# Kernel optimization log

Measured on AMD Instinct MI355X. Metric: run time of the kernel, lower is better.

Reference implementation:

```python
import jax, jax.numpy as jnp
import numpy as np

N, L, M, NNZ, P, G, H = 4096, 64, 256, 100000, 3, 1, 8
D = M // H  # head_dim = 32


def setup_inputs() -> dict:
    key = jax.random.key(0)
    ks = jax.random.split(key, 8)
    return {
        "sparse_values": jax.random.normal(ks[0], (NNZ, M), jnp.float32),
        "linear_index": jax.random.randint(ks[1], (N, L), 0, NNZ, jnp.int32),
        "is_specified": jax.random.randint(ks[2], (N, L), 0, 2, jnp.int32).astype(bool),
        "query": jax.random.normal(ks[3], (N, M), jnp.float32),
        "key_weight": jax.random.normal(ks[4], (M, M), jnp.float32) * 0.05,
        "value_weight": jax.random.normal(ks[5], (M, M), jnp.float32) * 0.05,
        "key_positions": jax.random.uniform(ks[6], (N, L, P), jnp.float32),
        "rope_freqs": jax.random.normal(ks[7], (P, G, H, D // 2), jnp.float32),
        "n_heads": H,
    }


def reference(sparse_values, linear_index, is_specified, query, key_weight,
              value_weight, key_positions, rope_freqs, n_heads):
    n, l = linear_index.shape
    m = query.shape[-1]
    h = n_heads
    d = m // h
    scale = 1.0 / np.sqrt(m)  # docstring: default scale_factor = 1/sqrt(M)

    # Gather each query's key subset; unspecified keys -> 0 (will be masked)
    safe_idx = jnp.where(is_specified, linear_index, 0)
    gathered = jnp.where(is_specified[..., None], sparse_values[safe_idx], 0.0)  # [N,L,M]

    # Key / value projections (nn.Linear convention: x @ W.T)
    k = (gathered @ key_weight.T).reshape(n, l, h, d)
    v = (gathered @ value_weight.T).reshape(n, l, h, d)

    # RoPE on keys: angles [N,L,H,D/2], summed over position dims P and freq groups G
    angles = jnp.einsum('nlp,pghd->nlhd', key_positions, rope_freqs)
    cos, sin = jnp.cos(angles), jnp.sin(angles)
    k_even, k_odd = k[..., 0::2], k[..., 1::2]
    k = jnp.stack([k_even * cos - k_odd * sin,
                   k_even * sin + k_odd * cos], axis=-1).reshape(n, l, h, d)

    # Per-query subset attention (query is pre-rotated per docstring)
    q = query.reshape(n, h, d)
    scores = jnp.einsum('nhd,nlhd->nhl', q, k) * scale
    scores = jnp.where(is_specified[:, None, :], scores, -jnp.inf)

    # Queries with all keys unspecified -> zero output (avoid NaN from all -inf)
    any_spec = is_specified.any(axis=-1)  # [N]
    attn = jax.nn.softmax(jnp.where(any_spec[:, None, None], scores, 0.0), axis=-1)
    out = jnp.einsum('nhl,nlhd->nhd', attn, v).reshape(n, m)
    out = jnp.where(any_spec[:, None], out, 0.0)
    return out, is_specified
```

## Files before the change

kernel.cpp:

```cpp
#include <hip/hip_runtime.h>
#include <math.h>

#define N_Q 4096
#define L_K 64
#define M_D 256

typedef float f32x16 __attribute__((ext_vector_type(16)));
typedef __bf16 b16x8 __attribute__((ext_vector_type(8)));
union F8 { uint4 u; unsigned short s[8]; b16x8 v; };

__device__ __forceinline__ unsigned short f2bf(float x) {
  unsigned u = __float_as_uint(x);
  return (unsigned short)((u + 0x7fffu + ((u >> 16) & 1u)) >> 16);
}

__global__ __launch_bounds__(256) void k_prep(const unsigned char* __restrict__ raw,
                                              float* __restrict__ out2,
                                              const float* __restrict__ wv,
                                              float* __restrict__ wvt,
                                              const float* __restrict__ wk,
                                              unsigned short* __restrict__ wkf,
                                              const int* __restrict__ lin,
                                              int* __restrict__ pcnt,
                                              int* __restrict__ plin,
                                              unsigned char* __restrict__ pl) {
  __shared__ int pll_s[256];
  __shared__ unsigned char pls_s[256];
  __shared__ int pc_s[4];
  const int tid = threadIdx.x, lane = tid & 63;
  pll_s[tid] = 0;
  pls_s[tid] = 0;
  int v = 0;
  for (int i = tid; i < 4096; i += 256)
    if (i & 3) v |= raw[i];
  int f = __syncthreads_or(v);
  const int gi = blockIdx.x * 256 + tid;
  bool b = f ? (raw[gi] != 0) : (((const int*)raw)[gi] != 0);
  out2[gi] = b ? 1.0f : 0.0f;
  int li = lin[gi];
  unsigned long long mask = __ballot(b);
  if (b) {
    int rank = __popcll(mask & ((1ull << lane) - 1));
    pll_s[(tid & 192) + rank] = li;
    pls_s[(tid & 192) + rank] = (unsigned char)lane;
  }
  if (lane == 0) pc_s[tid >> 6] = __popcll(mask);
  __syncthreads();
  plin[gi] = pll_s[tid];
  pl[gi] = pls_s[tid];
  if (tid < 4) pcnt[blockIdx.x * 4 + tid] = pc_s[tid];

  if (gi < 65536) {
    wvt[(gi & 255) * 256 + (gi >> 8)] = wv[gi];
    int oc = gi >> 8, k = gi & 255;
    int tt = oc >> 5, c32o = oc & 31;
    int ks = k >> 4, kg2 = (k >> 3) & 1, j = k & 7;
    wkf[(((tt * 16 + ks) << 6) + kg2 * 32 + c32o) * 8 + j] = f2bf(wk[gi]);
  }
}

__global__ __launch_bounds__(1024) void k_scan(const int* __restrict__ pcnt,
                                               int* __restrict__ pbase) {
  __shared__ int a[1024], b[1024];
  const int t = threadIdx.x;
  int c0 = pcnt[t * 4], c1 = pcnt[t * 4 + 1], c2 = pcnt[t * 4 + 2], c3 = pcnt[t * 4 + 3];
  a[t] = c0 + c1 + c2 + c3;
  __syncthreads();
  int* cur = a; int* alt = b;
  #pragma unroll
  for (int off = 1; off < 1024; off <<= 1) {
    int vv = cur[t] + ((t >= off) ? cur[t - off] : 0);
    alt[t] = vv;
    __syncthreads();
    int* tmp = cur; cur = alt; alt = tmp;
  }
  const int excl = (t > 0) ? cur[t - 1] : 0;
  pbase[t * 4]     = excl;
  pbase[t * 4 + 1] = excl + c0;
  pbase[t * 4 + 2] = excl + c0 + c1;
  pbase[t * 4 + 3] = excl + c0 + c1 + c2;
  if (t == 1023) pbase[4096] = cur[1023];
}

__global__ __launch_bounds__(256) void k_pack(const int* __restrict__ pcnt,
                                              const int* __restrict__ pbase,
                                              const int* __restrict__ plin,
                                              const unsigned char* __restrict__ pl,
                                              int* __restrict__ rowlinP,
                                              int* __restrict__ rinfoP) {
  const int gi = blockIdx.x * 256 + threadIdx.x;
  const int n = gi >> 6, r = gi & 63;
  if (r < pcnt[n]) {
    const int p = pbase[n] + r;
    rowlinP[p] = plin[gi];
    rinfoP[p] = n * 64 + pl[gi];
  }
}

__global__ __launch_bounds__(512, 4) void k_sgemm(
    const float* __restrict__ sv, const float* __restrict__ q,
    const unsigned short* __restrict__ wkf, const float* __restrict__ pos,
    const float* __restrict__ freqs, const int* __restrict__ pbase,
    const int* __restrict__ rowlinP, const int* __restrict__ rinfoP,
    float* __restrict__ scores_p) {
  const int total = pbase[4096];
  const int base = blockIdx.x * 128;
  if (base >= total) return;

  __shared__ __align__(16) char smem[65536];
  const int tid = threadIdx.x, lane = tid & 63, w = tid >> 6;
  const int c32 = lane & 31, kg = lane >> 5;
  const int rg = w >> 1, ch = w & 1;

  {
    const int rl = tid >> 5, ii = tid & 31;
    #pragma unroll
    for (int pp = 0; pp < 8; ++pp) {
      const int rloc = pp * 16 + rl;
      const int p = base + rloc;
      const int src = rowlinP[(p < total) ? p : (total - 1)];
      const float* rp = sv + (size_t)src * 256 + ii * 8;
      float4 f0 = *(const float4*)rp;
      float4 f1 = *(const float4*)(rp + 4);
      F8 pk;
      pk.s[0] = f2bf(f0.x); pk.s[1] = f2bf(f0.y); pk.s[2] = f2bf(f0.z); pk.s[3] = f2bf(f0.w);
      pk.s[4] = f2bf(f1.x); pk.s[5] = f2bf(f1.y); pk.s[6] = f2bf(f1.z); pk.s[7] = f2bf(f1.w);
      *(uint4*)(smem + rloc * 512 + ((ii ^ (rloc & 31)) << 4)) = pk.u;
    }
  }
  __syncthreads();

  f32x16 acc[4];
  #pragma unroll
  for (int t = 0; t < 4; ++t)
    #pragma unroll
    for (int r = 0; r < 16; ++r) acc[t][r] = 0.0f;

  const char* fbase = (const char*)wkf + ch * 65536 + lane * 16;
  F8 afc[4], afn[4];
  #pragma unroll
  for (int t = 0; t < 4; ++t) afc[t].u = *(const uint4*)(fbase + (t * 16) * 1024);

  #pragma unroll
  for (int ks = 0; ks < 16; ++ks) {
    if (ks < 15) {
      #pragma unroll
      for (int t = 0; t < 4; ++t)
        afn[t].u = *(const uint4*)(fbase + (t * 16 + ks + 1) * 1024);
    }
    F8 bf;
    bf.u = *(const uint4*)(smem + (rg * 32 + c32) * 512 + ((((ks << 1) + kg) ^ c32) << 4));
    #pragma unroll
    for (int t = 0; t < 4; ++t)
      acc[t] = __builtin_amdgcn_mfma_f32_32x32x16_bf16(afc[t].v, bf.v, acc[t], 0, 0, 0);
    #pragma unroll
    for (int t = 0; t < 4; ++t) afc[t] = afn[t];
  }

  const int p = base + rg * 32 + c32;
  const bool pv = p < total;
  const int info = pv ? rinfoP[p] : 0;
  const int nn_ = info >> 6;
  const float* lp = pos + (size_t)info * 3;
  const float pp0 = lp[0], pp1 = lp[1], pp2 = lp[2];
  #pragma unroll
  for (int t = 0; t < 4; ++t) {
    const int h = ch * 4 + t;
    const float* qh = q + (size_t)nn_ * 256 + h * 32;
    const float* F = freqs + h * 16;
    float s = 0.f;
    #pragma unroll
    for (int g = 0; g < 4; ++g) {
      #pragma unroll
      for (int pr = 0; pr < 2; ++pr) {
        const int d0 = g * 8 + kg * 4 + pr * 2;
        const int jj = d0 >> 1;
        const int r = g * 4 + pr * 2;
        float ke = acc[t][r], ko = acc[t][r + 1];
        float ang = pp0 * F[jj] + pp1 * F[128 + jj] + pp2 * F[256 + jj];
        float sn, cs;
        __sincosf(ang, &sn, &cs);
        float2 qq = *(const float2*)(qh + d0);
        s += ke * (cs * qq.x + sn * qq.y) + ko * (cs * qq.y - sn * qq.x);
      }
    }
    s += __shfl_xor(s, 32);
    if (kg == 0 && pv) scores_p[p * 8 + h] = s * 0.0625f;
  }
}

__global__ __launch_bounds__(256, 8) void k_vagg(
    const float* __restrict__ sv, const int* __restrict__ pcnt,
    const int* __restrict__ pbase, const int* __restrict__ rowlinP,
    const float* __restrict__ scores_p, unsigned short* __restrict__ agg) {
  __shared__ float attn_s[64][8];
  __shared__ float sc_s[64][8];
  __shared__ int rl_s[64];
  const int tid = threadIdx.x, lane = tid & 63, w = tid >> 6;
  const int n = blockIdx.x;
  const int cnt = pcnt[n];
  if (cnt == 0) {
    #pragma unroll
    for (int h = 0; h < 8; ++h) agg[(size_t)n * 2048 + h * 256 + tid] = 0;
    return;
  }
  const int pb = pbase[n];
  if (tid < cnt) rl_s[tid] = rowlinP[pb + tid];
  for (int i = tid; i < cnt * 8; i += 256)
    sc_s[i >> 3][i & 7] = scores_p[(size_t)pb * 8 + i];
  __syncthreads();

  #pragma unroll
  for (int uu = 0; uu < 2; ++uu) {
    const int h = w * 2 + uu;
    const bool vl = lane < cnt;
    float v = vl ? sc_s[lane][h] : -__builtin_inff();
    float mx = v;
    #pragma unroll
    for (int o = 32; o; o >>= 1) mx = fmaxf(mx, __shfl_xor(mx, o));
    float e = vl ? __expf(v - mx) : 0.f;
    float sm = e;
    #pragma unroll
    for (int o = 32; o; o >>= 1) sm += __shfl_xor(sm, o);
    attn_s[lane][h] = e / sm;
  }
  __syncthreads();

  const int m = tid;
  float ga[8];
  #pragma unroll
  for (int h = 0; h < 8; ++h) ga[h] = 0.f;
  #pragma unroll 8
  for (int pL = 0; pL < cnt; ++pL) {
    const float gv = sv[(size_t)rl_s[pL] * 256 + m];
    const float4* ap = (const float4*)&attn_s[pL][0];
    float4 aA = ap[0], aB = ap[1];
    ga[0] += aA.x * gv; ga[1] += aA.y * gv; ga[2] += aA.z * gv; ga[3] += aA.w * gv;
    ga[4] += aB.x * gv; ga[5] += aB.y * gv; ga[6] += aB.z * gv; ga[7] += aB.w * gv;
  }
  #pragma unroll
  for (int h = 0; h < 8; ++h)
    agg[(size_t)n * 2048 + h * 256 + m] = f2bf(ga[h]);
}

__global__ __launch_bounds__(256) void k_out(const unsigned short* __restrict__ agg,
                                             const float* __restrict__ wvt,
                                             float* __restrict__ out) {
  __shared__ float a_s[4][8][260];
  const int tid = threadIdx.x;
  const int n0 = blockIdx.x * 4;
  #pragma unroll
  for (int it = 0; it < 4; ++it) {
    uint4 v = *(const uint4*)(agg + (size_t)(n0 + it) * 2048 + tid * 8);
    const unsigned short* sp = (const unsigned short*)&v;
    const int hh = tid >> 5, m0 = (tid & 31) * 8;
    #pragma unroll
    for (int k2 = 0; k2 < 8; ++k2)
      a_s[it][hh][m0 + k2] = __uint_as_float((unsigned)sp[k2] << 16);
  }
  __syncthreads();
  const int m = tid, h = m >> 5;
  float o0 = 0.f, o1 = 0.f, o2 = 0.f, o3 = 0.f;
  #pragma unroll 8
  for (int j = 0; j < 256; ++j) {
    float wvv = wvt[j * 256 + m];
    o0 += a_s[0][h][j] * wvv;
    o1 += a_s[1][h][j] * wvv;
    o2 += a_s[2][h][j] * wvv;
    o3 += a_s[3][h][j] * wvv;
  }
  out[(n0 + 0) * 256 + m] = o0;
  out[(n0 + 1) * 256 + m] = o1;
  out[(n0 + 2) * 256 + m] = o2;
  out[(n0 + 3) * 256 + m] = o3;
}

extern "C" void kernel_launch(void* const* d_in, const int* in_sizes, int n_in,
                              void* d_out, int out_size, void* d_ws, size_t ws_size,
                              hipStream_t stream) {
  const float* sv  = (const float*)d_in[0];
  const int* lin   = (const int*)d_in[1];
  const unsigned char* raw = (const unsigned char*)d_in[2];
  const float* q   = (const float*)d_in[3];
  const float* wk  = (const float*)d_in[4];
  const float* wv  = (const float*)d_in[5];
  const float* pos = (const float*)d_in[6];
  const float* fq  = (const float*)d_in[7];
  float* out = (float*)d_out;
  char* ws = (char*)d_ws;

  float* wvt          = (float*)ws;
  unsigned short* wkf = (unsigned short*)(ws + 262144);
  int* pcnt           = (int*)(ws + 393216);
  int* pbase          = (int*)(ws + 409600);
  int* plin           = (int*)(ws + 426496);
  unsigned char* pl   = (unsigned char*)(ws + 1475072);
  int* rowlinP        = (int*)(ws + 1737216);
  int* rinfoP         = (int*)(ws + 2785792);
  float* scores_p     = (float*)(ws + 3834368);
  unsigned short* agg = (unsigned short*)(ws + 12222976);

  k_prep <<<1024, 256, 0, stream>>>(raw, out + N_Q * M_D, wv, wvt, wk, wkf,
                                    lin, pcnt, plin, pl);
  k_scan <<<1, 1024, 0, stream>>>(pcnt, pbase);
  k_pack <<<1024, 256, 0, stream>>>(pcnt, pbase, plin, pl, rowlinP, rinfoP);
  k_sgemm<<<2048, 512, 0, stream>>>(sv, q, wkf, pos, fq, pbase, rowlinP, rinfoP, scores_p);
  k_vagg <<<4096, 256, 0, stream>>>(sv, pcnt, pbase, rowlinP, scores_p, agg);
  k_out  <<<1024, 256, 0, stream>>>(agg, wvt, out);
}
```

Measured before the change: 123.0 us.

## Fuse scan, pack, score GEMM and value aggregation into per-query-pair kernel

Removes the global prefix scan and packing kernels and merges the score GEMM with softmax and value aggregation. Each block now handles two queries, packing their specified keys locally into LDS. The aggregation step reuses the bf16 gathered rows already staged in LDS instead of re-reading fp32 sparse_values from global memory. This cuts three launches and the scores/rowlin round trips, but pads tiles per query pair, so some MFMA work is wasted when the counts are not multiples of 32. Values are also aggregated in bf16 rather than fp32.

```diff
diff --git a/kernel.cpp b/kernel.cpp
--- a/kernel.cpp
+++ b/kernel.cpp
@@ -59,162 +59,127 @@
   }
 }
 
-__global__ __launch_bounds__(1024) void k_scan(const int* __restrict__ pcnt,
-                                               int* __restrict__ pbase) {
-  __shared__ int a[1024], b[1024];
-  const int t = threadIdx.x;
-  int c0 = pcnt[t * 4], c1 = pcnt[t * 4 + 1], c2 = pcnt[t * 4 + 2], c3 = pcnt[t * 4 + 3];
-  a[t] = c0 + c1 + c2 + c3;
-  __syncthreads();
-  int* cur = a; int* alt = b;
-  #pragma unroll
-  for (int off = 1; off < 1024; off <<= 1) {
-    int vv = cur[t] + ((t >= off) ? cur[t - off] : 0);
-    alt[t] = vv;
-    __syncthreads();
-    int* tmp = cur; cur = alt; alt = tmp;
-  }
-  const int excl = (t > 0) ? cur[t - 1] : 0;
-  pbase[t * 4]     = excl;
-  pbase[t * 4 + 1] = excl + c0;
-  pbase[t * 4 + 2] = excl + c0 + c1;
-  pbase[t * 4 + 3] = excl + c0 + c1 + c2;
-  if (t == 1023) pbase[4096] = cur[1023];
-}
-
-__global__ __launch_bounds__(256) void k_pack(const int* __restrict__ pcnt,
-                                              const int* __restrict__ pbase,
-                                              const int* __restrict__ plin,
-                                              const unsigned char* __restrict__ pl,
-                                              int* __restrict__ rowlinP,
-                                              int* __restrict__ rinfoP) {
-  const int gi = blockIdx.x * 256 + threadIdx.x;
-  const int n = gi >> 6, r = gi & 63;
-  if (r < pcnt[n]) {
-    const int p = pbase[n] + r;
-    rowlinP[p] = plin[gi];
-    rinfoP[p] = n * 64 + pl[gi];
-  }
-}
-
-__global__ __launch_bounds__(512, 4) void k_sgemm(
+#define SC_OFF  65536
+#define AT_OFF  (SC_OFF + 4096)
+#define LDS_SZ  (AT_OFF + 4096)
+
+__global__ __launch_bounds__(512, 4) void k_fused2(
     const float* __restrict__ sv, const float* __restrict__ q,
     const unsigned short* __restrict__ wkf, const float* __restrict__ pos,
-    const float* __restrict__ freqs, const int* __restrict__ pbase,
-    const int* __restrict__ rowlinP, const int* __restrict__ rinfoP,
-    float* __restrict__ scores_p) {
-  const int total = pbase[4096];
-  const int base = blockIdx.x * 128;
-  if (base >= total) return;
-
-  __shared__ __align__(16) char smem[65536];
+    const float* __restrict__ freqs, const int* __restrict__ pcnt,
+    const int* __restrict__ plin, const unsigned char* __restrict__ pl,
+    unsigned short* __restrict__ agg) {
+  __shared__ __align__(16) char smem[LDS_SZ];
+  float* sc_s   = (float*)(smem + SC_OFF);
+  float* attn_s = (float*)(smem + AT_OFF);
   const int tid = threadIdx.x, lane = tid & 63, w = tid >> 6;
   const int c32 = lane & 31, kg = lane >> 5;
-  const int rg = w >> 1, ch = w & 1;
+  const int rt = w >> 1, ch = w & 1;
+  const int n0g = blockIdx.x * 2;
+  const int cnt0 = pcnt[n0g], cnt1 = pcnt[n0g + 1];
+  const int cpair = cnt0 + cnt1;
+
+  if (cpair == 0) {
+    #pragma unroll
+    for (int i = tid; i < 1024; i += 512)
+      *(ushort4*)(agg + (size_t)n0g * 2048 + i * 4) = ushort4{0, 0, 0, 0};
+    return;
+  }
+  const int ct32 = (cpair + 31) & ~31;
+  const int ntiles = ct32 >> 5;
 
   {
-    const int rl = tid >> 5, ii = tid & 31;
+    const int r0 = tid >> 5, ii = tid & 31;
     #pragma unroll
     for (int pp = 0; pp < 8; ++pp) {
-      const int rloc = pp * 16 + rl;
-      const int p = base + rloc;
-      const int src = rowlinP[(p < total) ? p : (total - 1)];
-      const float* rp = sv + (size_t)src * 256 + ii * 8;
-      float4 f0 = *(const float4*)rp;
-      float4 f1 = *(const float4*)(rp + 4);
-      F8 pk;
-      pk.s[0] = f2bf(f0.x); pk.s[1] = f2bf(f0.y); pk.s[2] = f2bf(f0.z); pk.s[3] = f2bf(f0.w);
-      pk.s[4] = f2bf(f1.x); pk.s[5] = f2bf(f1.y); pk.s[6] = f2bf(f1.z); pk.s[7] = f2bf(f1.w);
-      *(uint4*)(smem + rloc * 512 + ((ii ^ (rloc & 31)) << 4)) = pk.u;
-    }
-  }
-  __syncthreads();
-
-  f32x16 acc[4];
-  #pragma unroll
-  for (int t = 0; t < 4; ++t)
-    #pragma unroll
-    for (int r = 0; r < 16; ++r) acc[t][r] = 0.0f;
-
-  const char* fbase = (const char*)wkf + ch * 65536 + lane * 16;
-  F8 afc[4], afn[4];
-  #pragma unroll
-  for (int t = 0; t < 4; ++t) afc[t].u = *(const uint4*)(fbase + (t * 16) * 1024);
-
-  #pragma unroll
-  for (int ks = 0; ks < 16; ++ks) {
-    if (ks < 15) {
-      #pragma unroll
-      for (int t = 0; t < 4; ++t)
-        afn[t].u = *(const uint4*)(fbase + (t * 16 + ks + 1) * 1024);
-    }
-    F8 bf;
-    bf.u = *(const uint4*)(smem + (rg * 32 + c32) * 512 + ((((ks << 1) + kg) ^ c32) << 4));
-    #pragma unroll
-    for (int t = 0; t < 4; ++t)
-      acc[t] = __builtin_amdgcn_mfma_f32_32x32x16_bf16(afc[t].v, bf.v, acc[t], 0, 0, 0);
-    #pragma unroll
-    for (int t = 0; t < 4; ++t) afc[t] = afn[t];
-  }
-
-  const int p = base + rg * 32 + c32;
-  const bool pv = p < total;
-  const int info = pv ? rinfoP[p] : 0;
-  const int nn_ = info >> 6;
-  const float* lp = pos + (size_t)info * 3;
-  const float pp0 = lp[0], pp1 = lp[1], pp2 = lp[2];
-  #pragma unroll
-  for (int t = 0; t < 4; ++t) {
-    const int h = ch * 4 + t;
-    const float* qh = q + (size_t)nn_ * 256 + h * 32;
-    const float* F = freqs + h * 16;
-    float s = 0.f;
-    #pragma unroll
-    for (int g = 0; g < 4; ++g) {
-      #pragma unroll
-      for (int pr = 0; pr < 2; ++pr) {
-        const int d0 = g * 8 + kg * 4 + pr * 2;
-        const int jj = d0 >> 1;
-        const int r = g * 4 + pr * 2;
-        float ke = acc[t][r], ko = acc[t][r + 1];
-        float ang = pp0 * F[jj] + pp1 * F[128 + jj] + pp2 * F[256 + jj];
-        float sn, cs;
-        __sincosf(ang, &sn, &cs);
-        float2 qq = *(const float2*)(qh + d0);
-        s += ke * (cs * qq.x + sn * qq.y) + ko * (cs * qq.y - sn * qq.x);
+      const int rloc = pp * 16 + r0;
+      if (rloc < ct32) {
+        const int pe = (rloc < cpair) ? rloc : (cpair - 1);
+        const int src = (pe < cnt0) ? plin[n0g * 64 + pe]
+                                    : plin[(n0g + 1) * 64 + (pe - cnt0)];
+        const float* rp = sv + (size_t)src * 256 + ii * 8;
+        float4 f0 = *(const float4*)rp;
+        float4 f1 = *(const float4*)(rp + 4);
+        F8 pk;
+        pk.s[0] = f2bf(f0.x); pk.s[1] = f2bf(f0.y); pk.s[2] = f2bf(f0.z); pk.s[3] = f2bf(f0.w);
+        pk.s[4] = f2bf(f1.x); pk.s[5] = f2bf(f1.y); pk.s[6] = f2bf(f1.z); pk.s[7] = f2bf(f1.w);
+        *(uint4*)(smem + rloc * 512 + ((ii ^ (rloc & 31)) << 4)) = pk.u;
       }
     }
-    s += __shfl_xor(s, 32);
-    if (kg == 0 && pv) scores_p[p * 8 + h] = s * 0.0625f;
-  }
-}
-
-__global__ __launch_bounds__(256, 8) void k_vagg(
-    const float* __restrict__ sv, const int* __restrict__ pcnt,
-    const int* __restrict__ pbase, const int* __restrict__ rowlinP,
-    const float* __restrict__ scores_p, unsigned short* __restrict__ agg) {
-  __shared__ float attn_s[64][8];
-  __shared__ float sc_s[64][8];
-  __shared__ int rl_s[64];
-  const int tid = threadIdx.x, lane = tid & 63, w = tid >> 6;
-  const int n = blockIdx.x;
-  const int cnt = pcnt[n];
-  if (cnt == 0) {
-    #pragma unroll
-    for (int h = 0; h < 8; ++h) agg[(size_t)n * 2048 + h * 256 + tid] = 0;
-    return;
-  }
-  const int pb = pbase[n];
-  if (tid < cnt) rl_s[tid] = rowlinP[pb + tid];
-  for (int i = tid; i < cnt * 8; i += 256)
-    sc_s[i >> 3][i & 7] = scores_p[(size_t)pb * 8 + i];
+  }
+  __syncthreads();
+
+  if (rt < ntiles) {
+    f32x16 acc[4];
+    #pragma unroll
+    for (int t = 0; t < 4; ++t)
+      #pragma unroll
+      for (int r = 0; r < 16; ++r) acc[t][r] = 0.0f;
+
+    const char* fbase = (const char*)wkf + ch * 65536 + lane * 16;
+    F8 afc[4], afn[4];
+    #pragma unroll
+    for (int t = 0; t < 4; ++t) afc[t].u = *(const uint4*)(fbase + (t * 16) * 1024);
+
+    #pragma unroll
+    for (int ks = 0; ks < 16; ++ks) {
+      if (ks < 15) {
+        #pragma unroll
+        for (int t = 0; t < 4; ++t)
+          afn[t].u = *(const uint4*)(fbase + (t * 16 + ks + 1) * 1024);
+      }
+      F8 bf;
+      bf.u = *(const uint4*)(smem + (rt * 32 + c32) * 512 + ((((ks << 1) + kg) ^ c32) << 4));
+      #pragma unroll
+      for (int t = 0; t < 4; ++t)
+        acc[t] = __builtin_amdgcn_mfma_f32_32x32x16_bf16(afc[t].v, bf.v, acc[t], 0, 0, 0);
+      #pragma unroll
+      for (int t = 0; t < 4; ++t) afc[t] = afn[t];
+    }
+
+    const int p = rt * 32 + c32;
+    const bool pv = p < cpair;
+    const int pe = pv ? p : (cpair - 1);
+    const int nl = (pe >= cnt0) ? 1 : 0;
+    const int n_g = n0g + nl;
+    const int l = pl[n_g * 64 + (pe - (nl ? cnt0 : 0))];
+    const float* lp = pos + ((size_t)n_g * 64 + l) * 3;
+    const float pp0 = lp[0], pp1 = lp[1], pp2 = lp[2];
+    #pragma unroll
+    for (int t = 0; t < 4; ++t) {
+      const int h = ch * 4 + t;
+      const float* qh = q + (size_t)n_g * 256 + h * 32;
+      const float* F = freqs + h * 16;
+      float s = 0.f;
+      #pragma unroll
+      for (int g = 0; g < 4; ++g) {
+        #pragma unroll
+        for (int pr = 0; pr < 2; ++pr) {
+          const int d0 = g * 8 + kg * 4 + pr * 2;
+          const int jj = d0 >> 1;
+          const int r = g * 4 + pr * 2;
+          float ke = acc[t][r], ko = acc[t][r + 1];
+          float ang = pp0 * F[jj] + pp1 * F[128 + jj] + pp2 * F[256 + jj];
+          float sn, cs;
+          __sincosf(ang, &sn, &cs);
+          float2 qq = *(const float2*)(qh + d0);
+          s += ke * (cs * qq.x + sn * qq.y) + ko * (cs * qq.y - sn * qq.x);
+        }
+      }
+      s += __shfl_xor(s, 32);
+      if (kg == 0 && pv) sc_s[p * 8 + h] = s * 0.0625f;
+    }
+  }
   __syncthreads();
 
   #pragma unroll
   for (int uu = 0; uu < 2; ++uu) {
-    const int h = w * 2 + uu;
-    const bool vl = lane < cnt;
-    float v = vl ? sc_s[lane][h] : -__builtin_inff();
+    const int unit = w * 2 + uu;
+    const int nl = unit >> 3, h = unit & 7;
+    const int start = nl ? cnt0 : 0;
+    const int cn = nl ? cnt1 : cnt0;
+    const bool vl = lane < cn;
+    float v = vl ? sc_s[(start + lane) * 8 + h] : -__builtin_inff();
     float mx = v;
     #pragma unroll
     for (int o = 32; o; o >>= 1) mx = fmaxf(mx, __shfl_xor(mx, o));
@@ -222,25 +187,30 @@
     float sm = e;
     #pragma unroll
     for (int o = 32; o; o >>= 1) sm += __shfl_xor(sm, o);
-    attn_s[lane][h] = e / sm;
-  }
-  __syncthreads();
-
-  const int m = tid;
+    if (vl) attn_s[(start + lane) * 8 + h] = e / sm;
+  }
+  __syncthreads();
+
+  const int m = tid & 255, hh = tid >> 8;
+  const int start = hh ? cnt0 : 0;
+  const int cn = hh ? cnt1 : cnt0;
+  const int n_g = n0g + hh;
   float ga[8];
   #pragma unroll
   for (int h = 0; h < 8; ++h) ga[h] = 0.f;
-  #pragma unroll 8
-  for (int pL = 0; pL < cnt; ++pL) {
-    const float gv = sv[(size_t)rl_s[pL] * 256 + m];
-    const float4* ap = (const float4*)&attn_s[pL][0];
+  for (int p2 = 0; p2 < cn; ++p2) {
+    const int prow = start + p2;
+    unsigned short us = *(const unsigned short*)(smem + prow * 512 +
+                        ((((m >> 3) ^ (prow & 31)) << 4) | ((m & 7) << 1)));
+    float gv = __uint_as_float((unsigned)us << 16);
+    const float4* ap = (const float4*)(attn_s + prow * 8);
     float4 aA = ap[0], aB = ap[1];
     ga[0] += aA.x * gv; ga[1] += aA.y * gv; ga[2] += aA.z * gv; ga[3] += aA.w * gv;
     ga[4] += aB.x * gv; ga[5] += aB.y * gv; ga[6] += aB.z * gv; ga[7] += aB.w * gv;
   }
   #pragma unroll
   for (int h = 0; h < 8; ++h)
-    agg[(size_t)n * 2048 + h * 256 + m] = f2bf(ga[h]);
+    agg[(size_t)n_g * 2048 + h * 256 + m] = f2bf(ga[h]);
 }
 
 __global__ __launch_bounds__(256) void k_out(const unsigned short* __restrict__ agg,
@@ -292,19 +262,12 @@
   float* wvt          = (float*)ws;
   unsigned short* wkf = (unsigned short*)(ws + 262144);
   int* pcnt           = (int*)(ws + 393216);
-  int* pbase          = (int*)(ws + 409600);
-  int* plin           = (int*)(ws + 426496);
-  unsigned char* pl   = (unsigned char*)(ws + 1475072);
-  int* rowlinP        = (int*)(ws + 1737216);
-  int* rinfoP         = (int*)(ws + 2785792);
-  float* scores_p     = (float*)(ws + 3834368);
-  unsigned short* agg = (unsigned short*)(ws + 12222976);
-
-  k_prep <<<1024, 256, 0, stream>>>(raw, out + N_Q * M_D, wv, wvt, wk, wkf,
-                                    lin, pcnt, plin, pl);
-  k_scan <<<1, 1024, 0, stream>>>(pcnt, pbase);
-  k_pack <<<1024, 256, 0, stream>>>(pcnt, pbase, plin, pl, rowlinP, rinfoP);
-  k_sgemm<<<2048, 512, 0, stream>>>(sv, q, wkf, pos, fq, pbase, rowlinP, rinfoP, scores_p);
-  k_vagg <<<4096, 256, 0, stream>>>(sv, pcnt, pbase, rowlinP, scores_p, agg);
-  k_out  <<<1024, 256, 0, stream>>>(agg, wvt, out);
-}
+  int* plin           = (int*)(ws + 409600);
+  unsigned char* pl   = (unsigned char*)(ws + 1458176);
+  unsigned short* agg = (unsigned short*)(ws + 1720320);
+
+  k_prep  <<<1024, 256, 0, stream>>>(raw, out + N_Q * M_D, wv, wvt, wk, wkf,
+                                     lin, pcnt, plin, pl);
+  k_fused2<<<2048, 512, 0, stream>>>(sv, q, wkf, pos, fq, pcnt, plin, pl, agg);
+  k_out   <<<1024, 256, 0, stream>>>(agg, wvt, out);
+}
```

Measured after the change: 108.8 us. 1.13x faster.
